# Kernel optimization log

Hardware: AMD Instinct MI355X
Metric: run time of the kernel (lower is better)

Reference implementation:

```python
import jax, jax.numpy as jnp
import numpy as np

# B batch, N seq (n_vec), V vocab, D model dim, H heads, DH head dim,
# L depth, WS window size, R landmark rank, C classes
B, N, V, D, H, DH, L, WS, R, C = 4, 4096, 512, 512, 8, 64, 4, 128, 256, 10
FF = 4 * D
SCALE = DH ** -0.5


def _ln(t, g, b, eps=1e-5):
    mu = jnp.mean(t, axis=-1, keepdims=True)
    var = jnp.var(t, axis=-1, keepdims=True)
    return (t - mu) * jax.lax.rsqrt(var + eps) * g + b


def setup_inputs():
    key = jax.random.key(0)
    ks = iter(jax.random.split(key, 16))

    def w(shape, s=0.02):
        return (jax.random.normal(next(ks), shape) * s).astype(jnp.float32)

    return dict(
        x=jax.random.randint(next(ks), (B, N), 0, V, dtype=jnp.int32),
        tok_emb=w((V, D)), pos_emb=w((N, D)),
        ln1_g=jnp.ones((L, D), jnp.float32), ln1_b=jnp.zeros((L, D), jnp.float32),
        Wq=w((L, D, H * DH)), Wkv=w((L, D, 2 * H * DH)), Wp=w((L, DH, R)),
        lln_g=jnp.ones((L, DH), jnp.float32), lln_b=jnp.zeros((L, DH), jnp.float32),
        gln_g=jnp.ones((L, DH), jnp.float32), gln_b=jnp.zeros((L, DH), jnp.float32),
        Wo=w((L, H * DH, D)), bo=jnp.zeros((L, D), jnp.float32),
        ln2_g=jnp.ones((L, D), jnp.float32), ln2_b=jnp.zeros((L, D), jnp.float32),
        W1=w((L, D, FF)), b1=jnp.zeros((L, FF), jnp.float32),
        W2=w((L, FF, D)), b2=jnp.zeros((L, D), jnp.float32),
        lnf_g=jnp.ones((D,), jnp.float32), lnf_b=jnp.zeros((D,), jnp.float32),
        Wlog=w((D, V)), blog=jnp.zeros((V,), jnp.float32),
        Wfin=w((N * V, C), 0.005), bfin=jnp.zeros((C,), jnp.float32),
    )


def _forward(x, tok_emb, pos_emb, ln1_g, ln1_b, Wq, Wkv, Wp, lln_g, lln_b,
             gln_g, gln_b, Wo, bo, ln2_g, ln2_b, W1, b1, W2, b2,
             lnf_g, lnf_b, Wlog, blog, Wfin, bfin):
    h = tok_emb[x] + pos_emb[None, :, :]  # [B,N,D]
    nw = N // WS
    for l in range(L):
        # ---- PreNorm Long-Short attention ----
        y = _ln(h, ln1_g[l], ln1_b[l])
        q = (y @ Wq[l]).reshape(B, N, H, DH).transpose(0, 2, 1, 3) * SCALE  # [B,H,N,DH]
        kv = (y @ Wkv[l]).reshape(B, N, 2, H, DH).transpose(2, 0, 3, 1, 4)
        k, v = kv[0], kv[1]  # [B,H,N,DH]
        # dynamic low-rank landmark projection: softmax over the sequence dim
        p = jax.nn.softmax(jnp.einsum('bhnd,dr->bhnr', k, Wp[l]), axis=2)
        gk = _ln(jnp.einsum('bhnr,bhnd->bhrd', p, k), gln_g[l], gln_b[l])  # [B,H,R,DH]
        gv = _ln(jnp.einsum('bhnr,bhnd->bhrd', p, v), gln_g[l], gln_b[l])
        # DualLN on the short-range (local window) keys/values
        lk = _ln(k, lln_g[l], lln_b[l]).reshape(B, H, nw, WS, DH)
        lv = _ln(v, lln_g[l], lln_b[l]).reshape(B, H, nw, WS, DH)
        lq = q.reshape(B, H, nw, WS, DH)
        sim_l = jnp.einsum('bhnwd,bhnxd->bhnwx', lq, lk)  # [B,H,nw,WS,WS]
        sim_g = jnp.einsum('bhnwd,bhrd->bhnwr', lq, gk)   # [B,H,nw,WS,R]
        attn = jax.nn.softmax(jnp.concatenate([sim_l, sim_g], axis=-1), axis=-1)
        a_l, a_g = attn[..., :WS], attn[..., WS:]
        o = (jnp.einsum('bhnwx,bhnxd->bhnwd', a_l, lv)
             + jnp.einsum('bhnwr,bhrd->bhnwd', a_g, gv))
        o = o.reshape(B, H, N, DH).transpose(0, 2, 1, 3).reshape(B, N, H * DH)
        h = h + o @ Wo[l] + bo[l]
        # ---- PreNorm FeedForward ----
        y = _ln(h, ln2_g[l], ln2_b[l])
        h = h + jax.nn.gelu(y @ W1[l] + b1[l]) @ W2[l] + b2[l]
    logits = _ln(h, lnf_g, lnf_b) @ Wlog + blog  # [B,N,V]
    # FLATTEN pooling head (dropout is identity in eval mode)
    return logits.reshape(B, N * V) @ Wfin + bfin  # [B,C]


def reference(x, tok_emb, pos_emb, ln1_g, ln1_b, Wq, Wkv, Wp, lln_g, lln_b,
              gln_g, gln_b, Wo, bo, ln2_g, ln2_b, W1, b1, W2, b2,
              lnf_g, lnf_b, Wlog, blog, Wfin, bfin):
    return _forward(x, tok_emb, pos_emb, ln1_g, ln1_b, Wq, Wkv, Wp, lln_g, lln_b,
                    gln_g, gln_b, Wo, bo, ln2_g, ln2_b, W1, b1, W2, b2,
                    lnf_g, lnf_b, Wlog, blog, Wfin, bfin)
```

## Files before the change

kernel.cpp:

```cpp
#include <hip/hip_runtime.h>
#include <hip/hip_bf16.h>

typedef unsigned short u16;
typedef __attribute__((ext_vector_type(8))) short short8;
typedef __attribute__((ext_vector_type(4))) float floatx4;

#define FLAG_GELU   1
#define FLAG_ACC    2
#define FLAG_NN     4
#define FLAG_CF32   8
#define FLAG_ATOMIC 16

__device__ __forceinline__ float bf2f(u16 u){
  union { unsigned u; float f; } c; c.u = ((unsigned)u)<<16; return c.f;
}
__device__ __forceinline__ u16 f2bf(float f){
  union { float f; unsigned u; } c; c.f = f;
  unsigned r = (c.u + 0x7fffu + ((c.u>>16)&1u))>>16;
  return (u16)r;
}
__device__ __forceinline__ float rdin(const void* base, long long idx, int flagv){
  return flagv ? ((const float*)base)[idx] : bf2f(((const u16*)base)[idx]);
}
__device__ __forceinline__ float fast_gelu(float x){
  float u = 0.7978845608028654f*(x + 0.044715f*x*x*x);
  float e = __expf(2.f*u);
  float t = 1.f - 2.f/(e+1.f);
  return 0.5f*x*(1.f+t);
}

__global__ void detect_kernel(const void* tok, int* flag){
  __shared__ int cnt;
  if(threadIdx.x==0) cnt=0;
  __syncthreads();
  float v = fabsf(bf2f(((const u16*)tok)[threadIdx.x]));
  int bad = (v < 1e3f) ? 0 : 1;
  atomicAdd(&cnt, bad);
  __syncthreads();
  if(threadIdx.x==0) *flag = (cnt>0) ? 1 : 0;
}

__global__ void cvtT_kernel(const void* src, long long off0, long long zstride, u16* __restrict__ dst,
    long long dzstride, int K, int N, const int* flag){
  __shared__ float tl[32][33];
  int fl = *flag;
  int k0 = blockIdx.x*32, n0 = blockIdx.y*32;
  long long base = off0 + (long long)blockIdx.z*zstride;
  for(int i=threadIdx.y;i<32;i+=8){
    long long idx = base + (long long)(k0+i)*N + n0 + threadIdx.x;
    tl[i][threadIdx.x] = fl ? ((const float*)src)[idx] : bf2f(((const u16*)src)[idx]);
  }
  __syncthreads();
  u16* dz = dst + (long long)blockIdx.z*dzstride;
  for(int i=threadIdx.y;i<32;i+=8)
    dz[(long long)(n0+i)*K + k0 + threadIdx.x] = f2bf(tl[threadIdx.x][i]);
}

__global__ void transposeB_kernel(const u16* __restrict__ in, u16* __restrict__ out,
    long long izs0, long long izs1, int zd, long long ozstride, int ldin, int ldout){
  __shared__ u16 tl[32][33];
  int z = blockIdx.z; int z0 = z/zd, z1 = z - z0*zd;
  const u16* ip = in + z0*izs0 + z1*izs1;
  u16* op = out + (long long)z*ozstride;
  int r0 = blockIdx.x*32, c0 = blockIdx.y*32;
  for(int i=threadIdx.y;i<32;i+=8)
    tl[i][threadIdx.x] = ip[(long long)(r0+i)*ldin + c0 + threadIdx.x];
  __syncthreads();
  for(int i=threadIdx.y;i<32;i+=8)
    op[(long long)(c0+i)*ldout + r0 + threadIdx.x] = tl[threadIdx.x][i];
}

__global__ __launch_bounds__(256) void zerof_kernel(float* p, int n){
  int i = blockIdx.x*256 + threadIdx.x;
  if(i<n) p[i]=0.f;
}

struct GemmP {
  const u16* A; const u16* B; float* Cf; u16* Ch;
  const void* bias; int biasOff; const int* dflag;
  int K, lda, ldb, ldc;
  long long sA0,sA1,sA2,sB0,sB1,sB2,sC0,sC1,sC2;
  int d0,d1; float alpha; int flags; int ksplit;
};

__global__ __launch_bounds__(256) void gemm_kernel(GemmP p){
  __shared__ __align__(16) u16 As[64][40];
  __shared__ __align__(16) u16 Bs[64][40];
  int z = blockIdx.z;
  int i0 = z / p.d0; int rem = z - i0*p.d0; int i1 = rem / p.d1; int i2 = rem - i1*p.d1;
  const u16* A  = p.A + i0*p.sA0 + i1*p.sA1 + i2*p.sA2;
  const u16* Bp = p.B + i0*p.sB0 + i1*p.sB1 + i2*p.sB2;
  long long cb = i0*p.sC0 + i1*p.sC1 + i2*p.sC2;
  int kbeg = 0, kend = p.K;
  if(p.ksplit){ kbeg = i2*p.ksplit; kend = kbeg + p.ksplit; }
  int m0 = blockIdx.x*64, n0 = blockIdx.y*64;
  int t = threadIdx.x, lane = t&63, wave = t>>6;
  int wm = (wave>>1)*32, wn = (wave&1)*32;
  int quad = lane>>4, l16 = lane&15;
  floatx4 zero4 = {0.f,0.f,0.f,0.f};
  floatx4 acc00=zero4, acc01=zero4, acc10=zero4, acc11=zero4;
  int sr = t>>2, sc = (t&3)*8;
  int bkr = t>>3, bnc = (t&7)*8;
  bool nn = (p.flags & FLAG_NN);
  for(int k0=kbeg;k0<kend;k0+=32){
    uint4 av = *(const uint4*)(A + (long long)(m0+sr)*p.lda + (k0+sc));
    uint4 bv;
    if(nn) bv = *(const uint4*)(Bp + (long long)(k0+bkr)*p.ldb + (n0+bnc));
    else   bv = *(const uint4*)(Bp + (long long)(n0+sr)*p.ldb + (k0+sc));
    *(uint4*)&As[sr][sc] = av;
    if(nn){
      u16 tmp[8]; *(uint4*)tmp = bv;
      #pragma unroll
      for(int j=0;j<8;j++) Bs[bnc+j][bkr] = tmp[j];
    } else {
      *(uint4*)&Bs[sr][sc] = bv;
    }
    __syncthreads();
    short8 a0 = *(const short8*)&As[wm+l16][quad*8];
    short8 a1 = *(const short8*)&As[wm+16+l16][quad*8];
    short8 b0 = *(const short8*)&Bs[wn+l16][quad*8];
    short8 b1 = *(const short8*)&Bs[wn+16+l16][quad*8];
    acc00 = __builtin_amdgcn_mfma_f32_16x16x32_bf16(a0,b0,acc00,0,0,0);
    acc01 = __builtin_amdgcn_mfma_f32_16x16x32_bf16(a0,b1,acc01,0,0,0);
    acc10 = __builtin_amdgcn_mfma_f32_16x16x32_bf16(a1,b0,acc10,0,0,0);
    acc11 = __builtin_amdgcn_mfma_f32_16x16x32_bf16(a1,b1,acc11,0,0,0);
    __syncthreads();
  }
  int flagv = p.bias ? *p.dflag : 0;
  #pragma unroll
  for(int mi=0;mi<2;mi++){
    #pragma unroll
    for(int ni=0;ni<2;ni++){
      floatx4 a = (mi==0)?((ni==0)?acc00:acc01):((ni==0)?acc10:acc11);
      int cg = n0 + wn + ni*16 + l16;
      float bv_ = p.bias ? rdin(p.bias, (long long)p.biasOff + cg, flagv) : 0.f;
      #pragma unroll
      for(int e=0;e<4;e++){
        int rg = m0 + wm + mi*16 + quad*4 + e;
        float v = a[e]*p.alpha + bv_;
        if(p.flags & FLAG_GELU) v = fast_gelu(v);
        long long ci = cb + (long long)rg*p.ldc + cg;
        if(p.flags & FLAG_ATOMIC){
          atomicAdd(&p.Cf[ci], v);
        } else if(p.flags & FLAG_CF32){
          float o2 = v; if(p.flags&FLAG_ACC) o2 += p.Cf[ci];
          p.Cf[ci] = o2;
        } else {
          float o2 = v; if(p.flags&FLAG_ACC) o2 += bf2f(p.Ch[ci]);
          p.Ch[ci] = f2bf(o2);
        }
      }
    }
  }
}

struct Gemm128P {
  const u16* A; const u16* B; float* Cf; u16* Ch;
  const void* bias; int biasOff; const int* dflag;
  int K, lda, ldb, ldc; float alpha; int flags;
};

template<int BM>
__global__ __launch_bounds__(512) void gemm2ph_kernel(Gemm128P p){
  constexpr int NA   = BM/64;
  constexpr int HH   = BM/2;
  constexpr int MI   = HH/16;
  constexpr int ABUF = BM*64;
  constexpr int LDSZ = (BM==256) ? 69632 : 49152;
  __shared__ __align__(16) u16 lds[LDSZ];
  u16* As = lds;
  u16* Bs = lds + 2*ABUF;
  int m0 = blockIdx.x*BM, n0 = blockIdx.y*256;
  int t = threadIdx.x, lane = t&63, wave = t>>6;
  int quad = lane>>4, l16 = lane&15;
  int wr = wave>>2, wc = wave&3;
  int rowA = t>>3;
  int colk = (((t&7) ^ (rowA&7)))*8;
  const u16* Asrc[NA];
  const u16* Bsrc[4];
  #pragma unroll
  for(int q=0;q<NA;q++) Asrc[q] = p.A + (long long)(m0 + q*64 + rowA)*p.lda + colk;
  #pragma unroll
  for(int q=0;q<4;q++)  Bsrc[q] = p.B + (long long)(n0 + q*64 + rowA)*p.ldb + colk;
  int nk = p.K >> 6;
  floatx4 acc[MI][4] = {};

  auto stage = [&](int buf, int k0){
    #pragma unroll
    for(int q=0;q<NA;q++)
      __builtin_amdgcn_global_load_lds(
        (const __attribute__((address_space(1))) unsigned int*)(Asrc[q] + k0),
        (__attribute__((address_space(3))) unsigned int*)(As + buf*ABUF + q*4096 + wave*512),
        16, 0, 0);
    #pragma unroll
    for(int q=0;q<4;q++)
      __builtin_amdgcn_global_load_lds(
        (const __attribute__((address_space(1))) unsigned int*)(Bsrc[q] + k0),
        (__attribute__((address_space(3))) unsigned int*)(Bs + buf*16384 + q*4096 + wave*512),
        16, 0, 0);
  };

  stage(0, 0);
  __syncthreads();
  int sw = l16&7;
  for(int kt=0; kt<nk; ++kt){
    int cur = kt&1;
    if(kt+1 < nk) stage(cur^1, (kt+1)*64);
    const u16* Ab = As + cur*ABUF;
    const u16* Bb = Bs + cur*16384;
    #pragma unroll
    for(int ks=0; ks<2; ks++){
      short8 a[MI], b[4];
      #pragma unroll
      for(int i=0;i<MI;i++)
        a[i] = *(const short8*)&Ab[(wr*HH + i*16 + l16)*64 + ((((ks<<2)|quad) ^ sw)<<3)];
      #pragma unroll
      for(int j=0;j<4;j++)
        b[j] = *(const short8*)&Bb[(wc*64 + j*16 + l16)*64 + ((((ks<<2)|quad) ^ sw)<<3)];
      #pragma unroll
      for(int i=0;i<MI;i++)
        #pragma unroll
        for(int j=0;j<4;j++)
          acc[i][j] = __builtin_amdgcn_mfma_f32_16x16x32_bf16(a[i], b[j], acc[i][j],0,0,0);
    }
    __syncthreads();
  }

  int flagv = p.bias ? *p.dflag : 0;
  if(!(p.flags & FLAG_CF32)){
    u16* Ct = lds + wave*(HH*68);
    #pragma unroll
    for(int j=0;j<4;j++){
      int cg = n0 + wc*64 + j*16 + l16;
      float bv_ = p.bias ? rdin(p.bias, (long long)p.biasOff + cg, flagv) : 0.f;
      #pragma unroll
      for(int i=0;i<MI;i++){
        #pragma unroll
        for(int e=0;e<4;e++){
          float v = acc[i][j][e]*p.alpha + bv_;
          if(p.flags & FLAG_GELU) v = fast_gelu(v);
          Ct[(i*16 + quad*4 + e)*68 + j*16 + l16] = f2bf(v);
        }
      }
    }
    int rsub = lane>>3, csub = (lane&7)*8;
    #pragma unroll
    for(int rr=0; rr<HH/8; rr++){
      int row = rr*8 + rsub;
      uint4 v = *(const uint4*)&Ct[row*68 + csub];
      *(uint4*)(p.Ch + (long long)(m0 + wr*HH + row)*p.ldc + (n0 + wc*64 + csub)) = v;
    }
  } else {
    #pragma unroll
    for(int j=0;j<4;j++){
      int cg = n0 + wc*64 + j*16 + l16;
      float bv_ = p.bias ? rdin(p.bias, (long long)p.biasOff + cg, flagv) : 0.f;
      #pragma unroll
      for(int i=0;i<MI;i++){
        #pragma unroll
        for(int e=0;e<4;e++){
          int rg = m0 + wr*HH + i*16 + quad*4 + e;
          float v = acc[i][j][e]*p.alpha + bv_;
          if(p.flags & FLAG_GELU) v = fast_gelu(v);
          long long ci = (long long)rg*p.ldc + cg;
          float o2 = v; if(p.flags&FLAG_ACC) o2 += p.Cf[ci];
          p.Cf[ci] = o2;
        }
      }
    }
  }
}

struct AttnP {
  const u16* q;
  const u16* k;
  const u16* gk;
  const u16* vT;
  const u16* gvT;
  u16* o;
};

__global__ __launch_bounds__(256) void attn_kernel(AttnP p){
  __shared__ __align__(16) u16 S[32*392];
  __shared__ float ssum[32];
  const int SST = 392;
  int qb = blockIdx.x;
  int bh = blockIdx.y;
  int b = bh>>3, hh = bh&7;
  int w = qb>>2;
  int t = threadIdx.x, lane = t&63, wave = t>>6;
  int quad = lane>>4, l16 = lane&15;
  int mbase = qb*32;
  short8 aq[2][2];
  #pragma unroll
  for(int mt=0;mt<2;mt++)
    #pragma unroll
    for(int kc=0;kc<2;kc++)
      aq[mt][kc] = *(const short8*)(p.q + ((long long)b*4096 + mbase + mt*16 + l16)*512 + hh*64 + kc*32 + quad*8);
  #pragma unroll
  for(int i=0;i<6;i++){
    int ct = wave*6 + i;
    short8 bf0, bf1;
    if(ct<8){
      const u16* kr = p.k + ((long long)b*4096 + w*128 + ct*16 + l16)*1024 + hh*64;
      bf0 = *(const short8*)(kr + quad*8);
      bf1 = *(const short8*)(kr + 32 + quad*8);
    } else {
      const u16* gr = p.gk + ((long long)bh*256 + (ct-8)*16 + l16)*64;
      bf0 = *(const short8*)(gr + quad*8);
      bf1 = *(const short8*)(gr + 32 + quad*8);
    }
    #pragma unroll
    for(int mt=0;mt<2;mt++){
      floatx4 acc = {0.f,0.f,0.f,0.f};
      acc = __builtin_amdgcn_mfma_f32_16x16x32_bf16(aq[mt][0], bf0, acc,0,0,0);
      acc = __builtin_amdgcn_mfma_f32_16x16x32_bf16(aq[mt][1], bf1, acc,0,0,0);
      #pragma unroll
      for(int e=0;e<4;e++)
        S[(mt*16 + quad*4 + e)*SST + ct*16 + l16] = f2bf(acc[e]);
    }
  }
  __syncthreads();
  {
    int r = t>>3, seg = t&7;
    u16* Srow = S + r*SST + seg*48;
    u16 buf[48];
    #pragma unroll
    for(int it=0; it<6; it++)
      *(uint4*)(buf + it*8) = *(const uint4*)(Srow + it*8);
    float mmax = -3.4e38f;
    #pragma unroll
    for(int j=0;j<48;j++) mmax = fmaxf(mmax, bf2f(buf[j]));
    mmax = fmaxf(mmax, __shfl_xor(mmax, 1));
    mmax = fmaxf(mmax, __shfl_xor(mmax, 2));
    mmax = fmaxf(mmax, __shfl_xor(mmax, 4));
    float s = 0.f;
    #pragma unroll
    for(int j=0;j<48;j++){ float e_ = __expf(bf2f(buf[j]) - mmax); s += e_; buf[j] = f2bf(e_); }
    #pragma unroll
    for(int it=0; it<6; it++)
      *(uint4*)(Srow + it*8) = *(const uint4*)(buf + it*8);
    s += __shfl_xor(s, 1);
    s += __shfl_xor(s, 2);
    s += __shfl_xor(s, 4);
    if(seg==0) ssum[r] = 1.f/s;
  }
  __syncthreads();
  int dt = wave;
  floatx4 oacc[2] = {};
  for(int kc=0; kc<12; kc++){
    short8 ap0 = *(const short8*)(S + (l16)*SST + kc*32 + quad*8);
    short8 ap1 = *(const short8*)(S + (16 + l16)*SST + kc*32 + quad*8);
    short8 bv;
    if(kc<4)
      bv = *(const short8*)(p.vT + (long long)bh*262144 + (dt*16+l16)*4096 + w*128 + kc*32 + quad*8);
    else
      bv = *(const short8*)(p.gvT + (long long)bh*16384 + (dt*16+l16)*256 + (kc-4)*32 + quad*8);
    oacc[0] = __builtin_amdgcn_mfma_f32_16x16x32_bf16(ap0, bv, oacc[0],0,0,0);
    oacc[1] = __builtin_amdgcn_mfma_f32_16x16x32_bf16(ap1, bv, oacc[1],0,0,0);
  }
  #pragma unroll
  for(int mt=0;mt<2;mt++){
    #pragma unroll
    for(int e=0;e<4;e++){
      int row = mt*16 + quad*4 + e;
      float inv = ssum[row];
      p.o[((long long)b*4096 + mbase + row)*512 + hh*64 + dt*16 + l16] = f2bf(oacc[mt][e]*inv);
    }
  }
}

__global__ __launch_bounds__(256) void embed_kernel(const int* __restrict__ x, const void* tok,
    const void* pos, float* __restrict__ h, const int* flag){
  int i = blockIdx.x*256 + threadIdx.x;
  int flagv = *flag;
  int d = i & 511;
  int n = (i>>9) & 4095;
  int bn = i>>9;
  int tid2 = x[bn];
  h[i] = rdin(tok, (long long)tid2*512 + d, flagv) + rdin(pos, (long long)n*512 + d, flagv);
}

__global__ __launch_bounds__(256) void ln512_kernel(const float* __restrict__ h,
    const void* g, const void* b, int goff, u16* __restrict__ y, const int* flag){
  int row = blockIdx.x;
  int flagv = *flag;
  const float* hr = h + (size_t)row*512;
  int t = threadIdx.x;
  float x0 = hr[t], x1 = hr[t+256];
  float s1 = x0+x1, s2 = x0*x0+x1*x1;
  for(int o=32;o>0;o>>=1){ s1 += __shfl_down(s1,o,64); s2 += __shfl_down(s2,o,64); }
  __shared__ float sh1[4], sh2[4];
  int wv=t>>6, ln=t&63;
  if(ln==0){ sh1[wv]=s1; sh2[wv]=s2; }
  __syncthreads();
  float st = sh1[0]+sh1[1]+sh1[2]+sh1[3];
  float qt = sh2[0]+sh2[1]+sh2[2]+sh2[3];
  float mu = st*(1.f/512.f);
  float var = qt*(1.f/512.f) - mu*mu;
  float inv = rsqrtf(var+1e-5f);
  u16* yr = y + (size_t)row*512;
  yr[t]     = f2bf((x0-mu)*inv*rdin(g,goff+t,flagv)     + rdin(b,goff+t,flagv));
  yr[t+256] = f2bf((x1-mu)*inv*rdin(g,goff+t+256,flagv) + rdin(b,goff+t+256,flagv));
}

__global__ __launch_bounds__(256) void ln64_kernel(const u16* __restrict__ in, const float* __restrict__ inF,
    u16* __restrict__ out, const void* g, const void* b, int goff,
    long long s0, long long s1v, long long s2v, int d0, int d1, const int* flag){
  int r = blockIdx.x*4 + (threadIdx.x>>6);
  int ln = threadIdx.x&63;
  int flagv = *flag;
  int i0 = r/d0; int rem = r - i0*d0; int i1 = rem/d1; int i2 = rem - i1*d1;
  long long off = i0*s0 + i1*s1v + i2*s2v;
  float x = inF ? inF[off+ln] : bf2f(in[off + ln]);
  float s = x, sq = x*x;
  for(int o=32;o>0;o>>=1){ s += __shfl_down(s,o,64); sq += __shfl_down(sq,o,64); }
  s = __shfl(s,0,64); sq = __shfl(sq,0,64);
  float mu = s*(1.f/64.f), var = sq*(1.f/64.f)-mu*mu;
  float inv = rsqrtf(var+1e-5f);
  out[off + ln] = f2bf((x-mu)*inv*rdin(g,goff+ln,flagv) + rdin(b,goff+ln,flagv));
}

__global__ __launch_bounds__(256) void softmax4096_kernel(u16* __restrict__ p){
  u16* pr = p + (size_t)blockIdx.x*4096;
  int t = threadIdx.x;
  u16 tmp[16];
  *(uint4*)tmp     = *(const uint4*)(pr + t*16);
  *(uint4*)(tmp+8) = *(const uint4*)(pr + t*16 + 8);
  float xs[16]; float m=-3.4e38f;
  #pragma unroll
  for(int i=0;i<16;i++){ xs[i]=bf2f(tmp[i]); m=fmaxf(m,xs[i]); }
  for(int o=32;o>0;o>>=1) m = fmaxf(m, __shfl_down(m,o,64));
  __shared__ float sm[4]; __shared__ float sv[4];
  int wv=t>>6, ln=t&63;
  if(ln==0) sm[wv]=m;
  __syncthreads();
  m = fmaxf(fmaxf(sm[0],sm[1]),fmaxf(sm[2],sm[3]));
  float s=0;
  #pragma unroll
  for(int i=0;i<16;i++){ xs[i]=__expf(xs[i]-m); s+=xs[i]; }
  for(int o=32;o>0;o>>=1) s += __shfl_down(s,o,64);
  if(ln==0) sv[wv]=s;
  __syncthreads();
  s = sv[0]+sv[1]+sv[2]+sv[3];
  float inv = 1.f/s;
  #pragma unroll
  for(int i=0;i<16;i++) tmp[i]=f2bf(xs[i]*inv);
  *(uint4*)(pr + t*16)     = *(uint4*)tmp;
  *(uint4*)(pr + t*16 + 8) = *(uint4*)(tmp+8);
}

__global__ void zero40_kernel(float* p){ if(threadIdx.x<40) p[threadIdx.x]=0.f; }

__global__ __launch_bounds__(256) void head_kernel(const float* __restrict__ logits,
    const void* wfin, float* __restrict__ part, const int* flag){
  __shared__ __align__(16) u16 Wl[20480];
  __shared__ float redl[4][40];
  int flagv = *flag;
  int t = threadIdx.x;
  long long rbase = (long long)blockIdx.x*2048;
  float acc[4][10];
  #pragma unroll
  for(int b4=0;b4<4;b4++)
    #pragma unroll
    for(int c=0;c<10;c++) acc[b4][c]=0.f;

  if(!flagv){
    const uint4* src = (const uint4*)((const u16*)wfin + rbase*10);
    uint4* dst = (uint4*)Wl;
    #pragma unroll
    for(int i=0;i<10;i++) dst[t + i*256] = src[t + i*256];
    __syncthreads();
    const unsigned* Wd = (const unsigned*)Wl;
    #pragma unroll
    for(int i=0;i<8;i++){
      int r = t + i*256;
      float l0 = logits[rbase + r];
      float l1 = logits[2097152 + rbase + r];
      float l2 = logits[4194304 + rbase + r];
      float l3 = logits[6291456 + rbase + r];
      #pragma unroll
      for(int k2=0;k2<5;k2++){
        unsigned d = Wd[r*5 + k2];
        float w0 = bf2f((u16)(d & 0xffffu));
        float w1 = bf2f((u16)(d >> 16));
        acc[0][2*k2]   += l0*w0; acc[0][2*k2+1] += l0*w1;
        acc[1][2*k2]   += l1*w0; acc[1][2*k2+1] += l1*w1;
        acc[2][2*k2]   += l2*w0; acc[2][2*k2+1] += l2*w1;
        acc[3][2*k2]   += l3*w0; acc[3][2*k2+1] += l3*w1;
      }
    }
  } else {
    #pragma unroll
    for(int i=0;i<8;i++){
      int r = t + i*256;
      float l0 = logits[rbase + r];
      float l1 = logits[2097152 + rbase + r];
      float l2 = logits[4194304 + rbase + r];
      float l3 = logits[6291456 + rbase + r];
      const float* wr = (const float*)wfin + (rbase + r)*10;
      #pragma unroll
      for(int c=0;c<10;c++){
        float w = wr[c];
        acc[0][c] += l0*w; acc[1][c] += l1*w; acc[2][c] += l2*w; acc[3][c] += l3*w;
      }
    }
  }
  int wv = t>>6, ln = t&63;
  #pragma unroll
  for(int b4=0;b4<4;b4++)
    #pragma unroll
    for(int c=0;c<10;c++){
      float v = acc[b4][c];
      for(int o=32;o>0;o>>=1) v += __shfl_down(v,o,64);
      if(ln==0) redl[wv][b4*10+c] = v;
    }
  __syncthreads();
  if(t<40) atomicAdd(&part[t], redl[0][t]+redl[1][t]+redl[2][t]+redl[3][t]);
}

__global__ void fin_kernel(const float* __restrict__ part, const void* bfin, void* out, const int* flag){
  int i=threadIdx.x;
  int flagv = *flag;
  if(i<40){
    float r = part[i] + rdin(bfin, i%10, flagv);
    if(flagv) ((float*)out)[i] = r;
    else      ((u16*)out)[i]   = f2bf(r);
  }
}

static const size_t OFF_H    = 0;
static const size_t OFF_Y    = 33554432;
static const size_t OFF_GKF  = 33554432;
static const size_t OFF_GVF  = 35651584;
static const size_t OFF_Q    = 50331648;
static const size_t OFF_KV   = 67108864;
static const size_t OFF_GK   = 100663296;
static const size_t OFF_GV   = 101711872;
static const size_t OFF_BIG  = 102760448;
static const size_t OFF_KT   = 169869312;
static const size_t OFF_VT   = 186646528;
static const size_t OFF_WTP  = 203423744;
static const size_t OFF_WQT  = 203554816;
static const size_t OFF_WKVT = 204079104;
static const size_t OFF_WOT  = 205127680;
static const size_t OFF_W1T  = 205651968;
static const size_t OFF_W2T  = 207749120;
static const size_t OFF_PART = 209846272;
static const size_t OFF_FLAG = 209846528;
static const size_t WS_NEED  = 209846784;

static inline GemmP mkg(const void*A,const void*B,void*C,const void*bias,int biasOff,const int* dflag,
  int K,int lda,int ldb,int ldc,
  long long a0,long long a1,long long a2,long long b0,long long b1,long long b2,
  long long c0,long long c1,long long c2,int d0,int d1,float alpha,int flags,int ksplit){
  GemmP p; p.A=(const u16*)A; p.B=(const u16*)B;
  p.Cf=(float*)C; p.Ch=(u16*)C; p.bias=bias; p.biasOff=biasOff; p.dflag=dflag;
  p.K=K;p.lda=lda;p.ldb=ldb;p.ldc=ldc;
  p.sA0=a0;p.sA1=a1;p.sA2=a2;p.sB0=b0;p.sB1=b1;p.sB2=b2;p.sC0=c0;p.sC1=c1;p.sC2=c2;
  p.d0=d0;p.d1=d1;p.alpha=alpha;p.flags=flags;p.ksplit=ksplit; return p;
}
static inline Gemm128P mk128(const void*A,const void*B,void*C,const void*bias,int biasOff,const int* dflag,
  int K,int lda,int ldb,int ldc,float alpha,int flags){
  Gemm128P p; p.A=(const u16*)A; p.B=(const u16*)B;
  p.Cf=(float*)C; p.Ch=(u16*)C; p.bias=bias; p.biasOff=biasOff; p.dflag=dflag;
  p.K=K;p.lda=lda;p.ldb=ldb;p.ldc=ldc;p.alpha=alpha;p.flags=flags; return p;
}

extern "C" void kernel_launch(void* const* d_in, const int* in_sizes, int n_in,
                              void* d_out, int out_size, void* d_ws, size_t ws_size,
                              hipStream_t stream){
  (void)in_sizes;(void)n_in;(void)out_size;
  if(ws_size < WS_NEED) return;
  const int*  x    = (const int*)d_in[0];
  const void* tok  = d_in[1];
  const void* pos  = d_in[2];
  const void* ln1g = d_in[3];
  const void* ln1b = d_in[4];
  const void* Wq   = d_in[5];
  const void* Wkv  = d_in[6];
  const void* Wp   = d_in[7];
  const void* llng = d_in[8];
  const void* llnb = d_in[9];
  const void* glng = d_in[10];
  const void* glnb = d_in[11];
  const void* Wo   = d_in[12];
  const void* bo   = d_in[13];
  const void* ln2g = d_in[14];
  const void* ln2b = d_in[15];
  const void* W1   = d_in[16];
  const void* b1   = d_in[17];
  const void* W2   = d_in[18];
  const void* b2   = d_in[19];
  const void* lnfg = d_in[20];
  const void* lnfb = d_in[21];
  const void* Wlog = d_in[22];
  const void* blog = d_in[23];
  const void* Wfin = d_in[24];
  const void* bfin = d_in[25];

  char* ws = (char*)d_ws;
  float* h    = (float*)(ws + OFF_H);
  u16* y      = (u16*)(ws + OFF_Y);
  u16* ob     = (u16*)(ws + OFF_Y);
  float* gkF  = (float*)(ws + OFF_GKF);
  float* gvF  = (float*)(ws + OFF_GVF);
  u16* qb     = (u16*)(ws + OFF_Q);
  u16* kv     = (u16*)(ws + OFF_KV);
  u16* gk     = (u16*)(ws + OFF_GK);
  u16* gv     = (u16*)(ws + OFF_GV);
  u16* big    = (u16*)(ws + OFF_BIG);
  float* bigf = (float*)(ws + OFF_BIG);
  u16* gvT    = (u16*)(ws + OFF_KT);
  u16* vT     = (u16*)(ws + OFF_VT);
  u16* wTp    = (u16*)(ws + OFF_WTP);
  u16* sWqT   = (u16*)(ws + OFF_WQT);
  u16* sWkvT  = (u16*)(ws + OFF_WKVT);
  u16* sWoT   = (u16*)(ws + OFF_WOT);
  u16* sW1T   = (u16*)(ws + OFF_W1T);
  u16* sW2T   = (u16*)(ws + OFF_W2T);
  float* part = (float*)(ws + OFF_PART);
  int* flag   = (int*)(ws + OFF_FLAG);

  dim3 tb(32,8);
  detect_kernel<<<dim3(1),dim3(256),0,stream>>>(tok, flag);
  cvtT_kernel<<<dim3(2,8,4),tb,0,stream>>>(Wp, 0, 16384, wTp, 16384, 64, 256, flag);
  embed_kernel<<<dim3(32768),dim3(256),0,stream>>>(x, tok, pos, h, flag);

  for(int l=0;l<4;l++){
    cvtT_kernel<<<dim3(16,16,1),tb,0,stream>>>(Wq,  (long long)l*262144,  0, sWqT,  0, 512, 512,  flag);
    cvtT_kernel<<<dim3(16,32,1),tb,0,stream>>>(Wkv, (long long)l*524288,  0, sWkvT, 0, 512, 1024, flag);
    cvtT_kernel<<<dim3(16,16,1),tb,0,stream>>>(Wo,  (long long)l*262144,  0, sWoT,  0, 512, 512,  flag);
    cvtT_kernel<<<dim3(16,64,1),tb,0,stream>>>(W1,  (long long)l*1048576, 0, sW1T,  0, 512, 2048, flag);
    cvtT_kernel<<<dim3(64,16,1),tb,0,stream>>>(W2,  (long long)l*1048576, 0, sW2T,  0, 2048, 512, flag);

    ln512_kernel<<<dim3(16384),dim3(256),0,stream>>>(h, ln1g, ln1b, l*512, y, flag);
    { Gemm128P p = mk128(y, sWqT, qb, nullptr,0,flag, 512,512,512,512, 0.125f, 0);
      gemm2ph_kernel<128><<<dim3(128,2),512,0,stream>>>(p); }
    { Gemm128P p = mk128(y, sWkvT, kv, nullptr,0,flag, 512,512,512,1024, 1.f, 0);
      gemm2ph_kernel<256><<<dim3(64,4),512,0,stream>>>(p); }
    zerof_kernel<<<dim3(4096),dim3(256),0,stream>>>(gkF, 1048576);
    { GemmP p = mkg(wTp + (size_t)l*16384, kv, big, nullptr,0,flag, 64,64,1024,4096,
        0,0,0, 4194304LL,64,0, 8388608LL,1048576LL,0, 8,1, 1.f, 0, 0);
      gemm_kernel<<<dim3(4,64,32),256,0,stream>>>(p); }
    softmax4096_kernel<<<dim3(8192),dim3(256),0,stream>>>(big);
    { GemmP p = mkg(big, kv, gkF, nullptr,0,flag, 4096,4096,1024,64,
        8388608LL,1048576LL,0, 4194304LL,64,0, 131072LL,16384LL,0, 64,8, 1.f,
        FLAG_CF32|FLAG_ATOMIC|FLAG_NN, 512);
      gemm_kernel<<<dim3(4,1,256),256,0,stream>>>(p); }
    { GemmP p = mkg(big, kv+512, gvF, nullptr,0,flag, 4096,4096,1024,64,
        8388608LL,1048576LL,0, 4194304LL,64,0, 131072LL,16384LL,0, 64,8, 1.f,
        FLAG_CF32|FLAG_ATOMIC|FLAG_NN, 512);
      gemm_kernel<<<dim3(4,1,256),256,0,stream>>>(p); }
    ln64_kernel<<<dim3(2048),dim3(256),0,stream>>>(gk, gkF, gk, glng, glnb, l*64, 64,1,1, 1,1, flag);
    ln64_kernel<<<dim3(2048),dim3(256),0,stream>>>(gv, gvF, gv, glng, glnb, l*64, 64,1,1, 1,1, flag);
    ln64_kernel<<<dim3(32768),dim3(256),0,stream>>>(kv,     nullptr, kv,     llng, llnb, l*64, 4194304LL,64,1024, 32768,4096, flag);
    ln64_kernel<<<dim3(32768),dim3(256),0,stream>>>(kv+512, nullptr, kv+512, llng, llnb, l*64, 4194304LL,64,1024, 32768,4096, flag);
    transposeB_kernel<<<dim3(128,2,32),tb,0,stream>>>(kv+512, vT, 4194304LL,64,8, 262144LL, 1024, 4096);
    transposeB_kernel<<<dim3(8,2,32),tb,0,stream>>>(gv, gvT, 16384LL,0,1, 16384LL, 64, 256);
    { AttnP ap; ap.q=qb; ap.k=kv; ap.gk=gk; ap.vT=vT; ap.gvT=gvT; ap.o=ob;
      attn_kernel<<<dim3(128,32),256,0,stream>>>(ap); }
    { Gemm128P p = mk128(ob, sWoT, h, bo,l*512,flag, 512,512,512,512, 1.f, FLAG_ACC|FLAG_CF32);
      gemm2ph_kernel<128><<<dim3(128,2),512,0,stream>>>(p); }
    ln512_kernel<<<dim3(16384),dim3(256),0,stream>>>(h, ln2g, ln2b, l*512, y, flag);
    { Gemm128P p = mk128(y, sW1T, big, b1,l*2048,flag, 512,512,512,2048, 1.f, FLAG_GELU);
      gemm2ph_kernel<256><<<dim3(64,8),512,0,stream>>>(p); }
    { Gemm128P p = mk128(big, sW2T, h, b2,l*512,flag, 2048,2048,2048,512, 1.f, FLAG_ACC|FLAG_CF32);
      gemm2ph_kernel<128><<<dim3(128,2),512,0,stream>>>(p); }
  }
  ln512_kernel<<<dim3(16384),dim3(256),0,stream>>>(h, lnfg, lnfb, 0, y, flag);
  cvtT_kernel<<<dim3(16,16,1),tb,0,stream>>>(Wlog, 0, 0, sWqT, 0, 512, 512, flag);
  { Gemm128P p = mk128(y, sWqT, bigf, blog,0,flag, 512,512,512,512, 1.f, FLAG_CF32);
    gemm2ph_kernel<128><<<dim3(128,2),512,0,stream>>>(p); }
  zero40_kernel<<<dim3(1),dim3(64),0,stream>>>(part);
  head_kernel<<<dim3(1024),dim3(256),0,stream>>>(bigf, Wfin, part, flag);
  fin_kernel<<<dim3(1),dim3(64),0,stream>>>(part, bfin, d_out, flag);
}
```

Baseline: 2.234 ms.

## Triple-buffer GEMM LDS staging with vmcnt-based waits and fixed 128-row tiles

Replaces the double-buffered templated GEMM with a triple-buffered 128x256 tile kernel. It prefetches two K-steps ahead and uses explicit s_waitcnt vmcnt counts plus raw barriers instead of __syncthreads, so global-to-LDS loads overlap more MFMA work. The BM=256 variants for the KV and W1 GEMMs become 128-row tiles with twice the grid. LDS use is 72KB, which may limit occupancy, and the hand-counted vmcnt values must match the number of outstanding loads exactly.

```diff
diff --git a/kernel.cpp b/kernel.cpp
--- a/kernel.cpp
+++ b/kernel.cpp
@@ -160,81 +160,85 @@
   int K, lda, ldb, ldc; float alpha; int flags;
 };
 
-template<int BM>
-__global__ __launch_bounds__(512) void gemm2ph_kernel(Gemm128P p){
-  constexpr int NA   = BM/64;
-  constexpr int HH   = BM/2;
-  constexpr int MI   = HH/16;
-  constexpr int ABUF = BM*64;
-  constexpr int LDSZ = (BM==256) ? 69632 : 49152;
-  __shared__ __align__(16) u16 lds[LDSZ];
-  u16* As = lds;
-  u16* Bs = lds + 2*ABUF;
-  int m0 = blockIdx.x*BM, n0 = blockIdx.y*256;
+__global__ __launch_bounds__(512) void gemm3b_kernel(Gemm128P p){
+  constexpr int TILE_A = 8192;
+  constexpr int TILE_B = 16384;
+  constexpr int TILE   = TILE_A + TILE_B;
+  __shared__ __align__(16) u16 lds[3*TILE];
+  int m0 = blockIdx.x*128, n0 = blockIdx.y*256;
   int t = threadIdx.x, lane = t&63, wave = t>>6;
   int quad = lane>>4, l16 = lane&15;
   int wr = wave>>2, wc = wave&3;
   int rowA = t>>3;
-  int colk = (((t&7) ^ (rowA&7)))*8;
-  const u16* Asrc[NA];
+  int colk = ((t&7) ^ (rowA&7))*8;
+  const u16* Asrc0 = p.A + (long long)(m0 + rowA)*p.lda + colk;
+  const u16* Asrc1 = p.A + (long long)(m0 + 64 + rowA)*p.lda + colk;
   const u16* Bsrc[4];
   #pragma unroll
-  for(int q=0;q<NA;q++) Asrc[q] = p.A + (long long)(m0 + q*64 + rowA)*p.lda + colk;
-  #pragma unroll
-  for(int q=0;q<4;q++)  Bsrc[q] = p.B + (long long)(n0 + q*64 + rowA)*p.ldb + colk;
+  for(int q=0;q<4;q++) Bsrc[q] = p.B + (long long)(n0 + q*64 + rowA)*p.ldb + colk;
   int nk = p.K >> 6;
-  floatx4 acc[MI][4] = {};
+  floatx4 acc[4][4] = {};
 
   auto stage = [&](int buf, int k0){
-    #pragma unroll
-    for(int q=0;q<NA;q++)
-      __builtin_amdgcn_global_load_lds(
-        (const __attribute__((address_space(1))) unsigned int*)(Asrc[q] + k0),
-        (__attribute__((address_space(3))) unsigned int*)(As + buf*ABUF + q*4096 + wave*512),
-        16, 0, 0);
+    u16* base = lds + buf*TILE;
+    __builtin_amdgcn_global_load_lds(
+      (const __attribute__((address_space(1))) unsigned int*)(Asrc0 + k0),
+      (__attribute__((address_space(3))) unsigned int*)(base + wave*512), 16, 0, 0);
+    __builtin_amdgcn_global_load_lds(
+      (const __attribute__((address_space(1))) unsigned int*)(Asrc1 + k0),
+      (__attribute__((address_space(3))) unsigned int*)(base + 4096 + wave*512), 16, 0, 0);
     #pragma unroll
     for(int q=0;q<4;q++)
       __builtin_amdgcn_global_load_lds(
         (const __attribute__((address_space(1))) unsigned int*)(Bsrc[q] + k0),
-        (__attribute__((address_space(3))) unsigned int*)(Bs + buf*16384 + q*4096 + wave*512),
-        16, 0, 0);
+        (__attribute__((address_space(3))) unsigned int*)(base + TILE_A + q*4096 + wave*512), 16, 0, 0);
   };
 
   stage(0, 0);
-  __syncthreads();
+  if(nk>1) stage(1, 64);
   int sw = l16&7;
   for(int kt=0; kt<nk; ++kt){
-    int cur = kt&1;
-    if(kt+1 < nk) stage(cur^1, (kt+1)*64);
-    const u16* Ab = As + cur*ABUF;
-    const u16* Bb = Bs + cur*16384;
+    if(kt+2<nk){
+      stage((kt+2)%3, (kt+2)*64);
+      asm volatile("s_waitcnt vmcnt(12)" ::: "memory");
+    } else if(kt+1<nk){
+      asm volatile("s_waitcnt vmcnt(6)" ::: "memory");
+    } else {
+      asm volatile("s_waitcnt vmcnt(0)" ::: "memory");
+    }
+    __builtin_amdgcn_s_barrier();
+    __builtin_amdgcn_sched_barrier(0);
+    const u16* Ab = lds + (kt%3)*TILE;
+    const u16* Bb = Ab + TILE_A;
     #pragma unroll
     for(int ks=0; ks<2; ks++){
-      short8 a[MI], b[4];
-      #pragma unroll
-      for(int i=0;i<MI;i++)
-        a[i] = *(const short8*)&Ab[(wr*HH + i*16 + l16)*64 + ((((ks<<2)|quad) ^ sw)<<3)];
+      short8 a[4], b[4];
+      #pragma unroll
+      for(int i=0;i<4;i++)
+        a[i] = *(const short8*)&Ab[(wr*64 + i*16 + l16)*64 + ((((ks<<2)|quad) ^ sw)<<3)];
       #pragma unroll
       for(int j=0;j<4;j++)
         b[j] = *(const short8*)&Bb[(wc*64 + j*16 + l16)*64 + ((((ks<<2)|quad) ^ sw)<<3)];
       #pragma unroll
-      for(int i=0;i<MI;i++)
+      for(int i=0;i<4;i++)
         #pragma unroll
         for(int j=0;j<4;j++)
           acc[i][j] = __builtin_amdgcn_mfma_f32_16x16x32_bf16(a[i], b[j], acc[i][j],0,0,0);
     }
-    __syncthreads();
+    __builtin_amdgcn_sched_barrier(0);
+    asm volatile("s_waitcnt lgkmcnt(0)" ::: "memory");
+    __builtin_amdgcn_s_barrier();
   }
 
   int flagv = p.bias ? *p.dflag : 0;
   if(!(p.flags & FLAG_CF32)){
-    u16* Ct = lds + wave*(HH*68);
+    u16* Ct = lds + wave*(64*68);
     #pragma unroll
     for(int j=0;j<4;j++){
       int cg = n0 + wc*64 + j*16 + l16;
       float bv_ = p.bias ? rdin(p.bias, (long long)p.biasOff + cg, flagv) : 0.f;
       #pragma unroll
-      for(int i=0;i<MI;i++){
+      for(int i=0;i<4;i++){
         #pragma unroll
         for(int e=0;e<4;e++){
           float v = acc[i][j][e]*p.alpha + bv_;
@@ -245,10 +249,10 @@
     }
     int rsub = lane>>3, csub = (lane&7)*8;
     #pragma unroll
-    for(int rr=0; rr<HH/8; rr++){
+    for(int rr=0; rr<8; rr++){
       int row = rr*8 + rsub;
       uint4 v = *(const uint4*)&Ct[row*68 + csub];
-      *(uint4*)(p.Ch + (long long)(m0 + wr*HH + row)*p.ldc + (n0 + wc*64 + csub)) = v;
+      *(uint4*)(p.Ch + (long long)(m0 + wr*64 + row)*p.ldc + (n0 + wc*64 + csub)) = v;
     }
   } else {
     #pragma unroll
@@ -256,10 +260,10 @@
       int cg = n0 + wc*64 + j*16 + l16;
       float bv_ = p.bias ? rdin(p.bias, (long long)p.biasOff + cg, flagv) : 0.f;
       #pragma unroll
-      for(int i=0;i<MI;i++){
+      for(int i=0;i<4;i++){
         #pragma unroll
         for(int e=0;e<4;e++){
-          int rg = m0 + wr*HH + i*16 + quad*4 + e;
+          int rg = m0 + wr*64 + i*16 + quad*4 + e;
           float v = acc[i][j][e]*p.alpha + bv_;
           if(p.flags & FLAG_GELU) v = fast_gelu(v);
           long long ci = (long long)rg*p.ldc + cg;
@@ -636,9 +640,9 @@
 
     ln512_kernel<<<dim3(16384),dim3(256),0,stream>>>(h, ln1g, ln1b, l*512, y, flag);
     { Gemm128P p = mk128(y, sWqT, qb, nullptr,0,flag, 512,512,512,512, 0.125f, 0);
-      gemm2ph_kernel<128><<<dim3(128,2),512,0,stream>>>(p); }
+      gemm3b_kernel<<<dim3(128,2),512,0,stream>>>(p); }
     { Gemm128P p = mk128(y, sWkvT, kv, nullptr,0,flag, 512,512,512,1024, 1.f, 0);
-      gemm2ph_kernel<256><<<dim3(64,4),512,0,stream>>>(p); }
+      gemm3b_kernel<<<dim3(128,4),512,0,stream>>>(p); }
     zerof_kernel<<<dim3(4096),dim3(256),0,stream>>>(gkF, 1048576);
     { GemmP p = mkg(wTp + (size_t)l*16384, kv, big, nullptr,0,flag, 64,64,1024,4096,
         0,0,0, 4194304LL,64,0, 8388608LL,1048576LL,0, 8,1, 1.f, 0, 0);
@@ -661,17 +665,17 @@
     { AttnP ap; ap.q=qb; ap.k=kv; ap.gk=gk; ap.vT=vT; ap.gvT=gvT; ap.o=ob;
       attn_kernel<<<dim3(128,32),256,0,stream>>>(ap); }
     { Gemm128P p = mk128(ob, sWoT, h, bo,l*512,flag, 512,512,512,512, 1.f, FLAG_ACC|FLAG_CF32);
-      gemm2ph_kernel<128><<<dim3(128,2),512,0,stream>>>(p); }
+      gemm3b_kernel<<<dim3(128,2),512,0,stream>>>(p); }
     ln512_kernel<<<dim3(16384),dim3(256),0,stream>>>(h, ln2g, ln2b, l*512, y, flag);
     { Gemm128P p = mk128(y, sW1T, big, b1,l*2048,flag, 512,512,512,2048, 1.f, FLAG_GELU);
-      gemm2ph_kernel<256><<<dim3(64,8),512,0,stream>>>(p); }
+      gemm3b_kernel<<<dim3(128,8),512,0,stream>>>(p); }
     { Gemm128P p = mk128(big, sW2T, h, b2,l*512,flag, 2048,2048,2048,512, 1.f, FLAG_ACC|FLAG_CF32);
-      gemm2ph_kernel<128><<<dim3(128,2),512,0,stream>>>(p); }
+      gemm3b_kernel<<<dim3(128,2),512,0,stream>>>(p); }
   }
   ln512_kernel<<<dim3(16384),dim3(256),0,stream>>>(h, lnfg, lnfb, 0, y, flag);
   cvtT_kernel<<<dim3(16,16,1),tb,0,stream>>>(Wlog, 0, 0, sWqT, 0, 512, 512, flag);
   { Gemm128P p = mk128(y, sWqT, bigf, blog,0,flag, 512,512,512,512, 1.f, FLAG_CF32);
-    gemm2ph_kernel<128><<<dim3(128,2),512,0,stream>>>(p); }
+    gemm3b_kernel<<<dim3(128,2),512,0,stream>>>(p); }
   zero40_kernel<<<dim3(1),dim3(64),0,stream>>>(part);
   head_kernel<<<dim3(1024),dim3(256),0,stream>>>(bigf, Wfin, part, flag);
   fin_kernel<<<dim3(1),dim3(64),0,stream>>>(part, bfin, d_out, flag);
```

After: 2.311 ms. +3.5%, slower.

## Fuse local V layernorm with transpose and swizzle GEMM workgroup order

Applied to the files above, without the earlier changes.

Replaces the separate in-place layernorm over the V half of kv and the following transpose into vT with one kernel that normalizes 32 rows per head in registers and writes the transposed result through LDS. This avoids a full read/write pass over V. Separately, the 2-phase GEMM remaps its workgroup index with an XCD-style modulo-8 swizzle so neighbouring tiles land on the same chiplet for better L2 reuse. The swizzle assumes the grid size is a multiple of 8. kv+512 is no longer normalized in place, so V is only ever used through vT.

```diff
diff --git a/kernel.cpp b/kernel.cpp
--- a/kernel.cpp
+++ b/kernel.cpp
@@ -68,6 +68,37 @@
   __syncthreads();
   for(int i=threadIdx.y;i<32;i+=8)
     op[(long long)(c0+i)*ldout + r0 + threadIdx.x] = tl[threadIdx.x][i];
+}
+
+__global__ __launch_bounds__(256) void lnT_kernel(const u16* __restrict__ kv, u16* __restrict__ vT,
+    const void* g, const void* b_, int goff, const int* flag){
+  __shared__ u16 tl[32][72];
+  int flagv = *flag;
+  int nt = blockIdx.x;
+  int bh = blockIdx.y;
+  int bb = bh>>3, hh = bh&7;
+  int t = threadIdx.x;
+  int r = t>>3, seg = t&7;
+  const u16* src = kv + (long long)bb*4194304 + (long long)(nt*32 + r)*1024 + 512 + hh*64 + seg*8;
+  u16 buf[8]; *(uint4*)buf = *(const uint4*)src;
+  float x[8]; float s=0.f, sq=0.f;
+  #pragma unroll
+  for(int j=0;j<8;j++){ x[j]=bf2f(buf[j]); s+=x[j]; sq+=x[j]*x[j]; }
+  s  += __shfl_xor(s,1);  s  += __shfl_xor(s,2);  s  += __shfl_xor(s,4);
+  sq += __shfl_xor(sq,1); sq += __shfl_xor(sq,2); sq += __shfl_xor(sq,4);
+  float mu = s*(1.f/64.f), var = sq*(1.f/64.f)-mu*mu;
+  float inv = rsqrtf(var+1e-5f);
+  #pragma unroll
+  for(int j=0;j<8;j++){
+    int d = seg*8+j;
+    tl[r][d] = f2bf((x[j]-mu)*inv*rdin(g,goff+d,flagv) + rdin(b_,goff+d,flagv));
+  }
+  __syncthreads();
+  int d = t>>2, nc = (t&3)*8;
+  u16 ob[8];
+  #pragma unroll
+  for(int j=0;j<8;j++) ob[j] = tl[nc+j][d];
+  *(uint4*)(vT + (long long)bh*262144 + (long long)d*4096 + nt*32 + nc) = *(uint4*)ob;
 }
 
 __global__ __launch_bounds__(256) void zerof_kernel(float* p, int n){
@@ -170,7 +201,12 @@
   __shared__ __align__(16) u16 lds[LDSZ];
   u16* As = lds;
   u16* Bs = lds + 2*ABUF;
-  int m0 = blockIdx.x*BM, n0 = blockIdx.y*256;
+  int gy = gridDim.y;
+  int nw = gridDim.x*gy;
+  int wg = blockIdx.x*gy + blockIdx.y;
+  int q8 = nw>>3;
+  int swz = (wg&7)*q8 + (wg>>3);
+  int m0 = (swz/gy)*BM, n0 = (swz - (swz/gy)*gy)*256;
   int t = threadIdx.x, lane = t&63, wave = t>>6;
   int quad = lane>>4, l16 = lane&15;
   int wr = wave>>2, wc = wave&3;
@@ -655,8 +691,7 @@
     ln64_kernel<<<dim3(2048),dim3(256),0,stream>>>(gk, gkF, gk, glng, glnb, l*64, 64,1,1, 1,1, flag);
     ln64_kernel<<<dim3(2048),dim3(256),0,stream>>>(gv, gvF, gv, glng, glnb, l*64, 64,1,1, 1,1, flag);
     ln64_kernel<<<dim3(32768),dim3(256),0,stream>>>(kv,     nullptr, kv,     llng, llnb, l*64, 4194304LL,64,1024, 32768,4096, flag);
-    ln64_kernel<<<dim3(32768),dim3(256),0,stream>>>(kv+512, nullptr, kv+512, llng, llnb, l*64, 4194304LL,64,1024, 32768,4096, flag);
-    transposeB_kernel<<<dim3(128,2,32),tb,0,stream>>>(kv+512, vT, 4194304LL,64,8, 262144LL, 1024, 4096);
+    lnT_kernel<<<dim3(128,32),dim3(256),0,stream>>>(kv, vT, llng, llnb, l*64, flag);
     transposeB_kernel<<<dim3(8,2,32),tb,0,stream>>>(gv, gvT, 16384LL,0,1, 16384LL, 64, 256);
     { AttnP ap; ap.q=qb; ap.k=kv; ap.gk=gk; ap.vT=vT; ap.gvT=gvT; ap.o=ob;
       attn_kernel<<<dim3(128,32),256,0,stream>>>(ap); }
```

Measured after the change: 2.191 ms. About the same (-1.9%).
